# Optimization experiments

Hardware: AMD Instinct MI355X
Metric: run time of the kernel (lower is better)

## Reference

```python
import jax, jax.numpy as jnp
import numpy as np

N = 50000      # nodes
E = 800000     # edges (before self-loops)
F_IN = 128     # num_node_features
G = 128        # number of graphs in batch
NEG_SLOPE = 0.2  # PyG GATConv leaky_relu slope


def _add_self_loops(src, dst, n):
    loop = jnp.arange(n, dtype=src.dtype)
    return jnp.concatenate([src, loop]), jnp.concatenate([dst, loop])


def gcn_conv(x, W, b, src, dst, n):
    h = x @ W
    deg = jax.ops.segment_sum(jnp.ones_like(dst, dtype=h.dtype), dst, num_segments=n)
    dinv = jnp.where(deg > 0, jax.lax.rsqrt(deg), 0.0)
    norm = dinv[src] * dinv[dst]                      # [E+N]
    msg = h[src] * norm[:, None]                      # gather + scale
    return jax.ops.segment_sum(msg, dst, num_segments=n) + b


def gat_conv(x, W, att_src, att_dst, b, src, dst, n, heads, ch):
    # PyG GATConv (concat=True, self-loops added by caller)
    h = (x @ W).reshape(n, heads, ch)                 # [N,H,C]
    a_src = (h * att_src).sum(-1)                     # [N,H]
    a_dst = (h * att_dst).sum(-1)                     # [N,H]
    e = jax.nn.leaky_relu(a_src[src] + a_dst[dst], NEG_SLOPE)  # [E+N,H]
    # segment softmax over edges grouped by destination
    m = jax.ops.segment_max(e, dst, num_segments=n)   # [N,H]
    ex = jnp.exp(e - m[dst])
    s = jax.ops.segment_sum(ex, dst, num_segments=n)  # [N,H]
    alpha = ex / s[dst]                               # [E+N,H]
    msg = h[src] * alpha[:, :, None]                  # [E+N,H,C]
    out = jax.ops.segment_sum(msg, dst, num_segments=n)
    return out.reshape(n, heads * ch) + b


def setup_inputs() -> dict:
    key = jax.random.key(0)
    ks = jax.random.split(key, 16)
    p = lambda k, shape: jax.random.normal(k, shape, jnp.float32) * 0.05
    return {
        "x": jax.random.normal(ks[0], (N, F_IN), jnp.float32),
        "edge_index": jax.random.randint(ks[1], (2, E), 0, N, dtype=jnp.int32),
        "batch": jnp.sort(jax.random.randint(ks[2], (N,), 0, G, dtype=jnp.int32)),
        "W1": p(ks[3], (F_IN, 16)), "b1": jnp.zeros((16,), jnp.float32),
        "W2": p(ks[4], (16, 32)), "b2": jnp.zeros((32,), jnp.float32),
        "W3": p(ks[5], (32, 4 * 32)), "att_src3": p(ks[6], (4, 32)), "att_dst3": p(ks[7], (4, 32)), "b3": jnp.zeros((128,), jnp.float32),
        "W4": p(ks[8], (128, 8 * 32)), "att_src4": p(ks[9], (8, 32)), "att_dst4": p(ks[10], (8, 32)), "b4": jnp.zeros((256,), jnp.float32),
        "Wfc1": p(ks[11], (432, 128)), "bfc1": jnp.zeros((128,), jnp.float32),
        "Wfc2": p(ks[12], (128, 1)), "bfc2": jnp.zeros((1,), jnp.float32),
    }


def reference(x, edge_index, batch, W1, b1, W2, b2, W3, att_src3, att_dst3, b3,
              W4, att_src4, att_dst4, b4, Wfc1, bfc1, Wfc2, bfc2):
    src, dst = _add_self_loops(edge_index[0], edge_index[1], N)
    x1 = jax.nn.relu(gcn_conv(x, W1, b1, src, dst, N))
    x2 = jax.nn.relu(gcn_conv(x1, W2, b2, src, dst, N))
    x3 = jax.nn.relu(gat_conv(x2, W3, att_src3, att_dst3, b3, src, dst, N, 4, 32))
    x4 = jax.nn.relu(gat_conv(x3, W4, att_src4, att_dst4, b4, src, dst, N, 8, 32))
    x_jump = jnp.concatenate([x1, x2, x3, x4], axis=-1)   # [N,432]
    # global mean pool over graphs
    sums = jax.ops.segment_sum(x_jump, batch, num_segments=G)
    cnt = jax.ops.segment_sum(jnp.ones((N,), x_jump.dtype), batch, num_segments=G)
    x_pool = sums / jnp.maximum(cnt, 1.0)[:, None]         # [G,432]
    h = jax.nn.relu(x_pool @ Wfc1 + bfc1)
    return (h @ Wfc2 + bfc2).flatten()                     # [G]
```

## Files before the change

kernel.cpp:

```cpp
#include <hip/hip_runtime.h>
#include <hip/hip_bf16.h>

#define NN 50000
#define NE 800000
#define NG 128
#define EB ((NE + 255)/256)
#define MB1 ((NN + 15)/16)
#define PB 54
#define WB4 128

typedef unsigned short u16;
typedef unsigned int u32;
typedef unsigned char u8;
typedef float f32x4 __attribute__((ext_vector_type(4)));
typedef short s16x8 __attribute__((ext_vector_type(8)));

__device__ __forceinline__ float lrelu(float x){ return x > 0.f ? x : 0.2f*x; }
__device__ __forceinline__ u16 f2bf(float f){
    __hip_bfloat16 h = __float2bfloat16(f);
    return *(u16*)&h;
}
__device__ __forceinline__ void unpack8(uint4 t, float* f){
    f[0]=__uint_as_float(t.x<<16); f[1]=__uint_as_float(t.x&0xffff0000u);
    f[2]=__uint_as_float(t.y<<16); f[3]=__uint_as_float(t.y&0xffff0000u);
    f[4]=__uint_as_float(t.z<<16); f[5]=__uint_as_float(t.z&0xffff0000u);
    f[6]=__uint_as_float(t.w<<16); f[7]=__uint_as_float(t.w&0xffff0000u);
}
__device__ __forceinline__ void ub8(uint2 t, float* f){
    f[0]=(float)(t.x & 0xffu);      f[1]=(float)((t.x>>8) & 0xffu);
    f[2]=(float)((t.x>>16) & 0xffu); f[3]=(float)(t.x>>24);
    f[4]=(float)(t.y & 0xffu);      f[5]=(float)((t.y>>8) & 0xffu);
    f[6]=(float)((t.y>>16) & 0xffu); f[7]=(float)(t.y>>24);
}

__global__ void k_cm(const int* __restrict__ dstE, int* __restrict__ degi,
                     const float* __restrict__ x, const float* __restrict__ W1,
                     const float* __restrict__ W3, const float* __restrict__ W4,
                     const float* __restrict__ as3, const float* __restrict__ ad3,
                     u16* __restrict__ h1, float* __restrict__ pool,
                     u16* __restrict__ W4p, float* __restrict__ asd3){
    if (blockIdx.x < EB){
        int e = blockIdx.x*256 + threadIdx.x;
        if (e < NE) atomicAdd(&degi[dstE[e]], 1);
        return;
    }
    if (blockIdx.x >= EB + MB1){
        int b2 = blockIdx.x - EB - MB1;
        if (b2 < PB){
            int idx = b2*1024 + threadIdx.x*4;
            if (idx < NG*432) *(float4*)(pool + idx) = make_float4(0.f,0.f,0.f,0.f);
        } else if (b2 < PB + WB4){
            int e = (b2 - PB)*256 + threadIdx.x;
            int k = e >> 8, n = e & 255;
            W4p[(k>>3)*2048 + n*8 + (k&7)] = f2bf(W4[e]);
        } else {
            int t = threadIdx.x;
            int t2 = t & 127;
            int h = t2 >> 5, k = t2 & 31;
            const float* av = (t < 128) ? as3 : ad3;
            float v = 0.f;
#pragma unroll
            for (int c = 0; c < 32; c++)
                v += W3[k*128 + h*32 + c] * av[h*32 + c];
            asd3[t] = v;
        }
        return;
    }
    __shared__ float wlT[16][132];
    __shared__ float xs[16][132];
    int node0 = (blockIdx.x - EB) * 16;
    for (int i = threadIdx.x; i < 2048; i += 256){
        int k = i >> 4, m = i & 15;
        wlT[m][k] = W1[i];
    }
    for (int i = threadIdx.x; i < 512; i += 256){
        int r = i >> 5, c = i & 31;
        *(float4*)&xs[r][c*4] = ((const float4*)(x + (size_t)(node0 + r)*128))[c];
    }
    __syncthreads();
    int m  = threadIdx.x & 15;
    int nl = threadIdx.x >> 4;
    float acc = 0.f;
#pragma unroll
    for (int k4 = 0; k4 < 32; k4++){
        float4 xv = *(const float4*)&xs[nl][k4*4];
        float4 wv = *(const float4*)&wlT[m][k4*4];
        acc += xv.x*wv.x + xv.y*wv.y + xv.z*wv.z + xv.w*wv.w;
    }
    h1[(size_t)(node0 + nl)*16 + m] = f2bf(acc);
}

__global__ void k_scan_a(const int* __restrict__ deg, int* __restrict__ rowptr,
                         float* __restrict__ dinv, int* __restrict__ cursor,
                         int* __restrict__ bsum, int n){
    __shared__ int lds[256];
    int base = blockIdx.x*1024 + threadIdx.x*4;
    int v[4]; int s = 0;
#pragma unroll
    for (int k=0;k<4;k++){ v[k] = (base+k < n) ? deg[base+k] : 0; s += v[k]; }
    lds[threadIdx.x] = s;
    __syncthreads();
    for (int off=1; off<256; off<<=1){
        int t = (threadIdx.x>=off) ? lds[threadIdx.x-off] : 0;
        __syncthreads(); lds[threadIdx.x] += t; __syncthreads();
    }
    int run = lds[threadIdx.x] - s;
#pragma unroll
    for (int k=0;k<4;k++){
        if (base+k < n){
            rowptr[base+k] = run;
            dinv[base+k] = rsqrtf((float)(v[k] + 1));
            cursor[base+k] = 0;
        }
        run += v[k];
    }
    if (threadIdx.x == 255) bsum[blockIdx.x] = lds[255];
}

__global__ void k_scan_c(int* __restrict__ rowptr, const int* __restrict__ bsum,
                         int nb, int n){
    __shared__ int off_s;
    if (threadIdx.x < 64){
        int v = ((int)threadIdx.x < nb && (int)threadIdx.x < (int)blockIdx.x)
                ? bsum[threadIdx.x] : 0;
        for (int m=1; m<64; m<<=1) v += __shfl_xor(v, m, 64);
        if (threadIdx.x == 0) off_s = v;
    }
    __syncthreads();
    int o = off_s;
    int idx = blockIdx.x*1024 + threadIdx.x*4;
#pragma unroll
    for (int k=0;k<4;k++) if (idx+k < n) rowptr[idx+k] += o;
    if ((int)blockIdx.x == nb-1 && threadIdx.x == 0) rowptr[n] = o + bsum[nb-1];
}

__global__ void k_scatter(const int* __restrict__ src, const int* __restrict__ dst,
                          const int* __restrict__ rowptr, int* __restrict__ cursor,
                          int* __restrict__ csr_src, int E){
    int e = blockIdx.x*blockDim.x + threadIdx.x;
    if (e < E){
        int d = dst[e];
        int pos = rowptr[d] + atomicAdd(&cursor[d], 1);
        csr_src[pos] = src[e];
    }
}

__global__ void k_gcn_agg16_mm2(const u16* __restrict__ h1, const float* __restrict__ dinv,
                                const int* __restrict__ rowptr, const int* __restrict__ csr_src,
                                const float* __restrict__ b1, const float* __restrict__ W2,
                                const int* __restrict__ batch, float* __restrict__ pool,
                                u16* __restrict__ h2, int n){
    __shared__ float w2s[16*32];
    __shared__ float x1s[16][17];
    __shared__ int gbuf[16];
    for (int i = threadIdx.x; i < 512; i += 256) w2s[i] = W2[i];
    int lin = threadIdx.x & 15;
    int nl  = threadIdx.x >> 4;
    int i = blockIdx.x*16 + nl;
    int ll = lin & 1, slot = lin >> 1;
    float di = dinv[i];
    float acc[8] = {0.f,0.f,0.f,0.f,0.f,0.f,0.f,0.f};
    if (slot == 0){
        uint4 t = *(const uint4*)(h1 + (size_t)i*16 + ll*8);
        float f[8]; unpack8(t, f);
#pragma unroll
        for (int k=0;k<8;k++) acc[k] = di*f[k];
    }
    int e0 = rowptr[i], e1 = rowptr[i+1];
    int e = e0 + slot;
    for (; e + 8 < e1; e += 16){
        int j0 = csr_src[e], j1 = csr_src[e+8];
        float d0 = dinv[j0], d1 = dinv[j1];
        uint4 t0 = *(const uint4*)(h1 + (size_t)j0*16 + ll*8);
        uint4 t1 = *(const uint4*)(h1 + (size_t)j1*16 + ll*8);
        float f0[8], f1[8]; unpack8(t0, f0); unpack8(t1, f1);
#pragma unroll
        for (int k=0;k<8;k++) acc[k] += d0*f0[k] + d1*f1[k];
    }
    if (e < e1){
        int j = csr_src[e];
        float dj = dinv[j];
        uint4 t = *(const uint4*)(h1 + (size_t)j*16 + ll*8);
        float f[8]; unpack8(t, f);
#pragma unroll
        for (int k=0;k<8;k++) acc[k] += dj*f[k];
    }
#pragma unroll
    for (int m = 2; m < 16; m <<= 1){
#pragma unroll
        for (int k=0;k<8;k++) acc[k] += __shfl_xor(acc[k], m, 64);
    }
    if (slot == 0){
#pragma unroll
        for (int k=0;k<8;k++)
            x1s[nl][ll*8+k] = fmaxf(di*acc[k] + b1[ll*8+k], 0.f);
        if (lin == 0) gbuf[nl] = batch[i];
    }
    __syncthreads();
    {
        float a0 = 0.f, a1 = 0.f;
        int m0 = lin*2;
#pragma unroll
        for (int k=0;k<16;k++){
            float xv = x1s[nl][k];
            a0 += xv * w2s[k*32 + m0];
            a1 += xv * w2s[k*32 + m0 + 1];
        }
        u32 pk = (u32)f2bf(a0) | ((u32)f2bf(a1) << 16);
        *(u32*)(h2 + (size_t)i*32 + m0) = pk;
    }
    if (threadIdx.x < 16){
        int c = threadIdx.x;
        int curg = gbuf[0];
        float a = 0.f;
        for (int nd = 0; nd < 16; nd++){
            int g = gbuf[nd];
            if (g != curg){ atomicAdd(&pool[curg*432 + c], a); a = 0.f; curg = g; }
            a += x1s[nd][c];
        }
        atomicAdd(&pool[curg*432 + c], a);
    }
}

__global__ void k_gcn_agg32(const u16* __restrict__ h2, const float* __restrict__ dinv,
                            const int* __restrict__ rowptr, const int* __restrict__ csr_src,
                            const float* __restrict__ b2, const int* __restrict__ batch,
                            const float* __restrict__ asd3, float* __restrict__ pool,
                            u16* __restrict__ x2b, float* __restrict__ asrc3,
                            float* __restrict__ adst3, int n){
    __shared__ float x2s[16][33];
    __shared__ float asdS[256];
    __shared__ int gbuf[16];
    asdS[threadIdx.x] = asd3[threadIdx.x];
    int lin = threadIdx.x & 15;
    int nl  = threadIdx.x >> 4;
    int i = blockIdx.x*16 + nl;
    int ll = lin & 3, slot = lin >> 2;
    float di = dinv[i];
    float acc[8] = {0.f,0.f,0.f,0.f,0.f,0.f,0.f,0.f};
    if (slot == 0){
        uint4 t = *(const uint4*)(h2 + (size_t)i*32 + ll*8);
        float f[8]; unpack8(t, f);
#pragma unroll
        for (int k=0;k<8;k++) acc[k] = di*f[k];
    }
    int e0 = rowptr[i], e1 = rowptr[i+1];
    int e = e0 + slot;
    for (; e + 12 < e1; e += 16){
        int j0 = csr_src[e], j1 = csr_src[e+4], j2 = csr_src[e+8], j3 = csr_src[e+12];
        float d0 = dinv[j0], d1 = dinv[j1], d2 = dinv[j2], d3 = dinv[j3];
        uint4 t0 = *(const uint4*)(h2 + (size_t)j0*32 + ll*8);
        uint4 t1 = *(const uint4*)(h2 + (size_t)j1*32 + ll*8);
        uint4 t2 = *(const uint4*)(h2 + (size_t)j2*32 + ll*8);
        uint4 t3 = *(const uint4*)(h2 + (size_t)j3*32 + ll*8);
        float f0[8], f1[8], f2[8], f3[8];
        unpack8(t0, f0); unpack8(t1, f1); unpack8(t2, f2); unpack8(t3, f3);
#pragma unroll
        for (int k=0;k<8;k++) acc[k] += d0*f0[k] + d1*f1[k] + d2*f2[k] + d3*f3[k];
    }
    for (; e < e1; e += 4){
        int j = csr_src[e];
        float dj = dinv[j];
        uint4 t = *(const uint4*)(h2 + (size_t)j*32 + ll*8);
        float f[8]; unpack8(t, f);
#pragma unroll
        for (int k=0;k<8;k++) acc[k] += dj*f[k];
    }
#pragma unroll
    for (int m = 4; m < 16; m <<= 1){
#pragma unroll
        for (int k=0;k<8;k++) acc[k] += __shfl_xor(acc[k], m, 64);
    }
    if (slot == 0){
        float o[8];
#pragma unroll
        for (int k=0;k<8;k++){
            o[k] = fmaxf(di*acc[k] + b2[ll*8+k], 0.f);
            x2s[nl][ll*8+k] = o[k];
        }
        uint4 pk;
        pk.x = (u32)f2bf(o[0]) | ((u32)f2bf(o[1])<<16);
        pk.y = (u32)f2bf(o[2]) | ((u32)f2bf(o[3])<<16);
        pk.z = (u32)f2bf(o[4]) | ((u32)f2bf(o[5])<<16);
        pk.w = (u32)f2bf(o[6]) | ((u32)f2bf(o[7])<<16);
        *(uint4*)(x2b + (size_t)i*32 + ll*8) = pk;
        if (lin == 0) gbuf[nl] = batch[i];
    }
    __syncthreads();
    if (threadIdx.x < 32){
        int c = threadIdx.x;
        int curg = gbuf[0];
        float a = 0.f;
        for (int nd = 0; nd < 16; nd++){
            int g = gbuf[nd];
            if (g != curg){ atomicAdd(&pool[curg*432 + 16 + c], a); a = 0.f; curg = g; }
            a += x2s[nd][c];
        }
        atomicAdd(&pool[curg*432 + 16 + c], a);
    } else if (threadIdx.x < 160){
        int t = threadIdx.x - 32;
        int nd = t >> 3, r = t & 7;
        int h = r & 3;
        const float* A = &asdS[(r >= 4 ? 128 : 0) + h*32];
        float v = 0.f;
#pragma unroll
        for (int k = 0; k < 32; k++) v += x2s[nd][k] * A[k];
        int node = blockIdx.x*16 + nd;
        if (r >= 4) adst3[(size_t)node*4 + h] = v;
        else        asrc3[(size_t)node*4 + h] = v;
    }
}

__global__ void k_gat_agg3(const u16* __restrict__ x2b, const float* __restrict__ asrc,
                           const float* __restrict__ adst, const int* __restrict__ rowptr,
                           const int* __restrict__ csr_src, const float* __restrict__ W3,
                           const float* __restrict__ b, const int* __restrict__ batch,
                           float* __restrict__ pool, u16* __restrict__ x3b, int n){
    __shared__ float W3s[32][128];
    __shared__ float aggS[4][4][32];
    __shared__ float x3s[4][128];
    __shared__ int gbuf[4];
    int tid = threadIdx.x;
    for (int idx = tid; idx < 4096; idx += 256)
        W3s[idx >> 7][idx & 127] = W3[idx];
    int lane = tid & 63;
    int wid  = tid >> 6;
    int i = blockIdx.x*4 + wid;
    int ll   = lane & 15;
    int slot = lane >> 4;
    int head = ll >> 2;
    int kseg = (ll & 3) * 8;
    float ad = adst[(size_t)i*4 + head];
    float acc[8] = {0.f,0.f,0.f,0.f,0.f,0.f,0.f,0.f};
    float s = 0.f;
    if (slot == 0){
        float w = __expf(lrelu(asrc[(size_t)i*4 + head] + ad));
        uint4 t = *(const uint4*)(x2b + (size_t)i*32 + kseg);
        float f[8]; unpack8(t, f);
#pragma unroll
        for (int k=0;k<8;k++) acc[k] = w*f[k];
        s = w;
    }
    int e0 = rowptr[i], e1 = rowptr[i+1];
    int e = e0 + slot;
    for (; e + 12 < e1; e += 16){
        int j0 = csr_src[e], j1 = csr_src[e+4], j2 = csr_src[e+8], j3 = csr_src[e+12];
        float w0 = __expf(lrelu(asrc[(size_t)j0*4 + head] + ad));
        float w1 = __expf(lrelu(asrc[(size_t)j1*4 + head] + ad));
        float w2 = __expf(lrelu(asrc[(size_t)j2*4 + head] + ad));
        float w3 = __expf(lrelu(asrc[(size_t)j3*4 + head] + ad));
        uint4 t0 = *(const uint4*)(x2b + (size_t)j0*32 + kseg);
        uint4 t1 = *(const uint4*)(x2b + (size_t)j1*32 + kseg);
        uint4 t2 = *(const uint4*)(x2b + (size_t)j2*32 + kseg);
        uint4 t3 = *(const uint4*)(x2b + (size_t)j3*32 + kseg);
        float f0[8], f1[8], f2[8], f3[8];
        unpack8(t0, f0); unpack8(t1, f1); unpack8(t2, f2); unpack8(t3, f3);
#pragma unroll
        for (int k=0;k<8;k++) acc[k] += w0*f0[k] + w1*f1[k] + w2*f2[k] + w3*f3[k];
        s += w0 + w1 + w2 + w3;
    }
    for (; e < e1; e += 4){
        int j = csr_src[e];
        float w = __expf(lrelu(asrc[(size_t)j*4 + head] + ad));
        uint4 t = *(const uint4*)(x2b + (size_t)j*32 + kseg);
        float f[8]; unpack8(t, f);
#pragma unroll
        for (int k=0;k<8;k++) acc[k] += w*f[k];
        s += w;
    }
#pragma unroll
    for (int m = 16; m < 64; m <<= 1){
        s += __shfl_xor(s, m, 64);
#pragma unroll
        for (int k=0;k<8;k++) acc[k] += __shfl_xor(acc[k], m, 64);
    }
    if (slot == 0){
        float inv = 1.f / s;
        float o[8];
#pragma unroll
        for (int k=0;k<8;k++) o[k] = acc[k]*inv;
        *(float4*)&aggS[wid][head][kseg]     = make_float4(o[0],o[1],o[2],o[3]);
        *(float4*)&aggS[wid][head][kseg + 4] = make_float4(o[4],o[5],o[6],o[7]);
        if (ll == 0) gbuf[wid] = batch[i];
    }
    __syncthreads();
    {
        int c0 = lane*2;
        const float* ag = aggS[wid][lane >> 4];
        float a0 = 0.f, a1 = 0.f;
#pragma unroll
        for (int k = 0; k < 32; k++){
            float av = ag[k];
            a0 += av * W3s[k][c0];
            a1 += av * W3s[k][c0+1];
        }
        float o0 = fmaxf(a0 + b[c0],   0.f);
        float o1 = fmaxf(a1 + b[c0+1], 0.f);
        x3s[wid][c0] = o0; x3s[wid][c0+1] = o1;
        u32 pk = (u32)f2bf(o0) | ((u32)f2bf(o1) << 16);
        *(u32*)(x3b + (size_t)i*128 + c0) = pk;
    }
    __syncthreads();
    if (tid < 128){
        int c = tid;
        int g0 = gbuf[0];
        float sum = 0.f;
#pragma unroll
        for (int wd = 0; wd < 4; wd++){
            float v = x3s[wd][c];
            int gw = gbuf[wd];
            if (gw == g0) sum += v;
            else atomicAdd(&pool[gw*432 + 48 + c], v);
        }
        atomicAdd(&pool[g0*432 + 48 + c], sum);
    }
}

__global__ void k_mm4_mfma(const u16* __restrict__ x3b, const u16* __restrict__ W4p,
                           const float* __restrict__ as, const float* __restrict__ adt,
                           u8* __restrict__ hb, float* __restrict__ scl,
                           float* __restrict__ asrc, float* __restrict__ adst){
    __shared__ u16 outS[64][136];
    __shared__ float asS[128], adS[128];
    int tid = threadIdx.x;
    int lane = tid & 63, w = tid >> 6;
    int cbase = blockIdx.x * 128;
    int nbase = blockIdx.y * 64;
    if (tid < 128){ asS[tid] = as[cbase + tid]; adS[tid] = adt[cbase + tid]; }
    int q = lane >> 4, r16 = lane & 15;
    int m = nbase + w*16 + r16;
    f32x4 acc[8] = {};
    for (int s = 0; s < 4; s++){
        s16x8 af = (s16x8){0,0,0,0,0,0,0,0};
        if (m < NN) af = *(const s16x8*)(x3b + (size_t)m*128 + s*32 + q*8);
        int kb = s*4 + q;
#pragma unroll
        for (int t = 0; t < 8; t++){
            s16x8 bf = *(const s16x8*)(W4p + (size_t)kb*2048 + (cbase + t*16 + r16)*8);
            acc[t] = __builtin_amdgcn_mfma_f32_16x16x32_bf16(af, bf, acc[t], 0, 0, 0);
        }
    }
#pragma unroll
    for (int t = 0; t < 8; t++){
#pragma unroll
        for (int r = 0; r < 4; r++){
            outS[w*16 + q*4 + r][t*16 + r16] = f2bf(acc[t][r]);
        }
    }
    __syncthreads();
    {
        int row = w*16 + r16;
        int node = nbase + row;
        float ps = 0.f, pd = 0.f, mx = 0.f;
        const u16* orow = &outS[row][q*32];
#pragma unroll
        for (int c = 0; c < 32; c++){
            float f = __uint_as_float(((u32)orow[c]) << 16);
            ps += f * asS[q*32 + c];
            pd += f * adS[q*32 + c];
            mx = fmaxf(mx, fabsf(f));
        }
        if (node < NN){
            int hg = (cbase >> 5) + q;
            asrc[(size_t)node*8 + hg] = ps;
            adst[(size_t)node*8 + hg] = pd;
        }
        mx = fmaxf(mx, __shfl_xor(mx, 16, 64));
        mx = fmaxf(mx, __shfl_xor(mx, 32, 64));
        float inv = mx > 0.f ? 127.f/mx : 0.f;
        if (node < NN && q == 0) scl[(size_t)node*2 + (cbase>>7)] = mx * (1.f/127.f);
        if (node < NN){
            u32 pk_[8];
#pragma unroll
            for (int g = 0; g < 8; g++){
                u32 v = 0;
#pragma unroll
                for (int kk = 0; kk < 4; kk++){
                    float f = __uint_as_float(((u32)orow[g*4+kk]) << 16);
                    int bq = (int)rintf(f*inv) + 128;
                    v |= ((u32)bq) << (8*kk);
                }
                pk_[g] = v;
            }
            *(uint4*)(hb + (size_t)node*256 + cbase + q*32)      = make_uint4(pk_[0],pk_[1],pk_[2],pk_[3]);
            *(uint4*)(hb + (size_t)node*256 + cbase + q*32 + 16) = make_uint4(pk_[4],pk_[5],pk_[6],pk_[7]);
        }
    }
}

__global__ void k_gat_agg4(const u8* __restrict__ h, const float* __restrict__ scl,
                           const float* __restrict__ asrc, const float* __restrict__ adst,
                           const int* __restrict__ rowptr, const int* __restrict__ csr_src,
                           const float* __restrict__ b, const int* __restrict__ batch,
                           float* __restrict__ pool){
    constexpr int S = 2;
    __shared__ float x4buf[4][256];
    __shared__ int gbuf[4];
    int lane = threadIdx.x & 63;
    int wid  = threadIdx.x >> 6;
    int i = blockIdx.x*4 + wid;
    int ll   = lane & 31;
    int slot = lane >> 5;
    int head = ll >> 2;
    int half = ll >> 4;
    float ad = adst[(size_t)i*8 + head];
    float acc[8] = {0.f,0.f,0.f,0.f,0.f,0.f,0.f,0.f};
    float s = 0.f, cw = 0.f;
    if (slot == 0){
        float w = __expf(lrelu(asrc[(size_t)i*8 + head] + ad));
        float ws = w * scl[(size_t)i*2 + half];
        uint2 t = *(const uint2*)(h + (size_t)i*256 + ll*8);
        float f[8]; ub8(t, f);
#pragma unroll
        for (int k=0;k<8;k++) acc[k] = ws*f[k];
        s = w; cw = ws;
    }
    int e0 = rowptr[i], e1 = rowptr[i+1];
    int e = e0 + slot;
    for (; e + 3*S < e1; e += 4*S){
        int j0 = csr_src[e], j1 = csr_src[e+S], j2 = csr_src[e+2*S], j3 = csr_src[e+3*S];
        float w0 = __expf(lrelu(asrc[(size_t)j0*8 + head] + ad));
        float w1 = __expf(lrelu(asrc[(size_t)j1*8 + head] + ad));
        float w2 = __expf(lrelu(asrc[(size_t)j2*8 + head] + ad));
        float w3 = __expf(lrelu(asrc[(size_t)j3*8 + head] + ad));
        float ws0 = w0 * scl[(size_t)j0*2 + half];
        float ws1 = w1 * scl[(size_t)j1*2 + half];
        float ws2 = w2 * scl[(size_t)j2*2 + half];
        float ws3 = w3 * scl[(size_t)j3*2 + half];
        uint2 t0 = *(const uint2*)(h + (size_t)j0*256 + ll*8);
        uint2 t1 = *(const uint2*)(h + (size_t)j1*256 + ll*8);
        uint2 t2 = *(const uint2*)(h + (size_t)j2*256 + ll*8);
        uint2 t3 = *(const uint2*)(h + (size_t)j3*256 + ll*8);
        float f0[8], f1[8], f2[8], f3[8];
        ub8(t0, f0); ub8(t1, f1); ub8(t2, f2); ub8(t3, f3);
#pragma unroll
        for (int k=0;k<8;k++) acc[k] += ws0*f0[k] + ws1*f1[k] + ws2*f2[k] + ws3*f3[k];
        s += w0 + w1 + w2 + w3;
        cw += ws0 + ws1 + ws2 + ws3;
    }
    for (; e < e1; e += S){
        int j = csr_src[e];
        float w = __expf(lrelu(asrc[(size_t)j*8 + head] + ad));
        float ws = w * scl[(size_t)j*2 + half];
        uint2 t = *(const uint2*)(h + (size_t)j*256 + ll*8);
        float f[8]; ub8(t, f);
#pragma unroll
        for (int k=0;k<8;k++) acc[k] += ws*f[k];
        s += w; cw += ws;
    }
#pragma unroll
    for (int k=0;k<8;k++) acc[k] -= 128.f*cw;
    s += __shfl_xor(s, 32, 64);
#pragma unroll
    for (int k=0;k<8;k++) acc[k] += __shfl_xor(acc[k], 32, 64);
    if (slot == 0){
        float inv = 1.f / s;
#pragma unroll
        for (int k=0;k<8;k++)
            x4buf[wid][ll*8+k] = fmaxf(acc[k]*inv + b[ll*8+k], 0.f);
        if (ll == 0) gbuf[wid] = batch[i];
    }
    __syncthreads();
    {
        int c = threadIdx.x;
        int g0 = gbuf[0];
        float sum = 0.f;
#pragma unroll
        for (int wd = 0; wd < 4; wd++){
            float v = x4buf[wd][c];
            int gw = gbuf[wd];
            if (gw == g0) sum += v;
            else atomicAdd(&pool[gw*432 + 176 + c], v);
        }
        atomicAdd(&pool[g0*432 + 176 + c], sum);
    }
}

__global__ void k_fc(const float* __restrict__ pool, const int* __restrict__ batch,
                     const float* __restrict__ Wf1, const float* __restrict__ bf1,
                     const float* __restrict__ Wf2, const float* __restrict__ bf2,
                     float* __restrict__ out){
    int g = blockIdx.x, j = threadIdx.x;
    int lo = 0, hi = NN;
    while (lo < hi){ int mid = (lo+hi) >> 1; if (batch[mid] < g) lo = mid+1; else hi = mid; }
    int s0 = lo;
    lo = 0; hi = NN;
    while (lo < hi){ int mid = (lo+hi) >> 1; if (batch[mid] < g+1) lo = mid+1; else hi = mid; }
    int cnt = lo - s0;
    float invc = 1.f / (float)max(cnt, 1);
    float acc = 0.f;
    for (int k = 0; k < 432; k++) acc += pool[g*432 + k] * Wf1[k*128 + j];
    float hv = fmaxf(acc * invc + bf1[j], 0.f);
    float p = hv * Wf2[j];
    for (int off = 32; off > 0; off >>= 1) p += __shfl_down(p, off, 64);
    __shared__ float part[2];
    if ((j & 63) == 0) part[j >> 6] = p;
    __syncthreads();
    if (j == 0) out[g] = part[0] + part[1] + bf2[0];
}

extern "C" void kernel_launch(void* const* d_in, const int* in_sizes, int n_in,
                              void* d_out, int out_size, void* d_ws, size_t ws_size,
                              hipStream_t stream){
    const float* x     = (const float*)d_in[0];
    const int*   ei    = (const int*)  d_in[1];
    const int*   batch = (const int*)  d_in[2];
    const float* W1 = (const float*)d_in[3];  const float* b1 = (const float*)d_in[4];
    const float* W2 = (const float*)d_in[5];  const float* b2 = (const float*)d_in[6];
    const float* W3 = (const float*)d_in[7];
    const float* as3 = (const float*)d_in[8]; const float* ad3 = (const float*)d_in[9];
    const float* b3 = (const float*)d_in[10];
    const float* W4 = (const float*)d_in[11];
    const float* as4 = (const float*)d_in[12]; const float* ad4 = (const float*)d_in[13];
    const float* b4 = (const float*)d_in[14];
    const float* Wf1 = (const float*)d_in[15]; const float* bf1 = (const float*)d_in[16];
    const float* Wf2 = (const float*)d_in[17]; const float* bf2 = (const float*)d_in[18];
    float* out = (float*)d_out;

    const int* srcE = ei;
    const int* dstE = ei + NE;

    char* base = (char*)d_ws; size_t off = 0;
    auto alloc = [&](size_t bytes)->void*{
        void* p = base + off;
        off += (bytes + 255) & ~(size_t)255;
        return p;
    };
    int*   degi    = (int*)  alloc((size_t)NN*4);
    int*   cursor  = (int*)  alloc((size_t)NN*4);
    float* dinv    = (float*)alloc((size_t)NN*4);
    int*   rowptr  = (int*)  alloc((size_t)(NN+1)*4);
    int*   bsum    = (int*)  alloc(64*4);
    int*   csr_src = (int*)  alloc((size_t)NE*4);
    u16*   h1b     = (u16*)  alloc((size_t)NN*16*2);
    u16*   h2b     = (u16*)  alloc((size_t)NN*32*2);
    u8*    hb4     = (u8*)   alloc((size_t)NN*256);
    float* scl4    = (float*)alloc((size_t)NN*2*4);
    u16*   x2b     = (u16*)  alloc((size_t)NN*32*2);
    u16*   x3b     = (u16*)  alloc((size_t)NN*128*2);
    u16*   W4p     = (u16*)  alloc((size_t)32768*2);
    float* asd3    = (float*)alloc(256*4);
    float* a_src   = (float*)alloc((size_t)NN*8*4);
    float* a_dst   = (float*)alloc((size_t)NN*8*4);
    float* pool    = (float*)alloc((size_t)NG*432*4);

    hipMemsetAsync(degi, 0, (size_t)NN*4, stream);

    const int SB = (NN + 1023)/1024;

    k_cm     <<<EB + MB1 + PB + WB4 + 1, 256, 0, stream>>>(dstE, degi, x, W1, W3, W4,
                                                           as3, ad3, h1b, pool, W4p, asd3);
    k_scan_a <<<SB, 256, 0, stream>>>(degi, rowptr, dinv, cursor, bsum, NN);
    k_scan_c <<<SB, 256, 0, stream>>>(rowptr, bsum, SB, NN);
    k_scatter<<<EB, 256, 0, stream>>>(srcE, dstE, rowptr, cursor, csr_src, NE);

    k_gcn_agg16_mm2<<<NN/16, 256, 0, stream>>>(h1b, dinv, rowptr, csr_src, b1, W2,
                                               batch, pool, h2b, NN);

    k_gcn_agg32<<<NN/16, 256, 0, stream>>>(h2b, dinv, rowptr, csr_src, b2, batch,
                                           asd3, pool, x2b, a_src, a_dst, NN);

    k_gat_agg3<<<NN/4, 256, 0, stream>>>(x2b, a_src, a_dst, rowptr, csr_src, W3, b3,
                                         batch, pool, x3b, NN);

    {
        dim3 grid(2, (NN + 63)/64);
        k_mm4_mfma<<<grid, 256, 0, stream>>>(x3b, W4p, as4, ad4, hb4, scl4, a_src, a_dst);
    }
    k_gat_agg4<<<NN/4, 256, 0, stream>>>(hb4, scl4, a_src, a_dst, rowptr, csr_src, b4,
                                         batch, pool);

    k_fc<<<NG, 128, 0, stream>>>(pool, batch, Wf1, bf1, Wf2, bf2, out);
}
```

Measured before the change: 375.0 us.

## Process four nodes per wave in GAT layer-3 aggregation to amortize W3 staging

Each wave now handles four destination nodes sequentially instead of one, so each block covers 16 nodes and the grid shrinks fourfold. This amortizes the 16KB W3 shared-memory load across more nodes. The per-node aggregated vector is broadcast through wave shuffles rather than a shared buffer, which removes the two block barriers after the gather. Pooling is reduced per wave in registers before the atomics. In exchange there are fewer blocks and the four nodes in a wave run serially, which may lower the number of gathers in flight at once.

```diff
diff --git a/kernel.cpp b/kernel.cpp
--- a/kernel.cpp
+++ b/kernel.cpp
@@ -317,103 +317,99 @@
                            const float* __restrict__ b, const int* __restrict__ batch,
                            float* __restrict__ pool, u16* __restrict__ x3b, int n){
     __shared__ float W3s[32][128];
-    __shared__ float aggS[4][4][32];
-    __shared__ float x3s[4][128];
-    __shared__ int gbuf[4];
     int tid = threadIdx.x;
     for (int idx = tid; idx < 4096; idx += 256)
         W3s[idx >> 7][idx & 127] = W3[idx];
+    __syncthreads();
     int lane = tid & 63;
     int wid  = tid >> 6;
-    int i = blockIdx.x*4 + wid;
     int ll   = lane & 15;
     int slot = lane >> 4;
     int head = ll >> 2;
     int kseg = (ll & 3) * 8;
-    float ad = adst[(size_t)i*4 + head];
-    float acc[8] = {0.f,0.f,0.f,0.f,0.f,0.f,0.f,0.f};
-    float s = 0.f;
-    if (slot == 0){
-        float w = __expf(lrelu(asrc[(size_t)i*4 + head] + ad));
-        uint4 t = *(const uint4*)(x2b + (size_t)i*32 + kseg);
-        float f[8]; unpack8(t, f);
-#pragma unroll
-        for (int k=0;k<8;k++) acc[k] = w*f[k];
-        s = w;
-    }
-    int e0 = rowptr[i], e1 = rowptr[i+1];
-    int e = e0 + slot;
-    for (; e + 12 < e1; e += 16){
-        int j0 = csr_src[e], j1 = csr_src[e+4], j2 = csr_src[e+8], j3 = csr_src[e+12];
-        float w0 = __expf(lrelu(asrc[(size_t)j0*4 + head] + ad));
-        float w1 = __expf(lrelu(asrc[(size_t)j1*4 + head] + ad));
-        float w2 = __expf(lrelu(asrc[(size_t)j2*4 + head] + ad));
-        float w3 = __expf(lrelu(asrc[(size_t)j3*4 + head] + ad));
-        uint4 t0 = *(const uint4*)(x2b + (size_t)j0*32 + kseg);
-        uint4 t1 = *(const uint4*)(x2b + (size_t)j1*32 + kseg);
-        uint4 t2 = *(const uint4*)(x2b + (size_t)j2*32 + kseg);
-        uint4 t3 = *(const uint4*)(x2b + (size_t)j3*32 + kseg);
-        float f0[8], f1[8], f2[8], f3[8];
-        unpack8(t0, f0); unpack8(t1, f1); unpack8(t2, f2); unpack8(t3, f3);
-#pragma unroll
-        for (int k=0;k<8;k++) acc[k] += w0*f0[k] + w1*f1[k] + w2*f2[k] + w3*f3[k];
-        s += w0 + w1 + w2 + w3;
-    }
-    for (; e < e1; e += 4){
-        int j = csr_src[e];
-        float w = __expf(lrelu(asrc[(size_t)j*4 + head] + ad));
-        uint4 t = *(const uint4*)(x2b + (size_t)j*32 + kseg);
-        float f[8]; unpack8(t, f);
-#pragma unroll
-        for (int k=0;k<8;k++) acc[k] += w*f[k];
-        s += w;
-    }
-#pragma unroll
-    for (int m = 16; m < 64; m <<= 1){
-        s += __shfl_xor(s, m, 64);
-#pragma unroll
-        for (int k=0;k<8;k++) acc[k] += __shfl_xor(acc[k], m, 64);
-    }
-    if (slot == 0){
+    int c0   = lane * 2;
+    int ph   = lane >> 4;
+    float bc0 = b[c0], bc1 = b[c0+1];
+    float o_r[4][2];
+    int   g_r[4];
+    int ibase = blockIdx.x * 16 + wid * 4;
+#pragma unroll
+    for (int t = 0; t < 4; t++){
+        int i = ibase + t;
+        float ad = adst[(size_t)i*4 + head];
+        float acc[8] = {0.f,0.f,0.f,0.f,0.f,0.f,0.f,0.f};
+        float s = 0.f;
+        if (slot == 0){
+            float w = __expf(lrelu(asrc[(size_t)i*4 + head] + ad));
+            uint4 tq = *(const uint4*)(x2b + (size_t)i*32 + kseg);
+            float f[8]; unpack8(tq, f);
+#pragma unroll
+            for (int k=0;k<8;k++) acc[k] = w*f[k];
+            s = w;
+        }
+        int e0 = rowptr[i], e1 = rowptr[i+1];
+        int e = e0 + slot;
+        for (; e + 12 < e1; e += 16){
+            int j0 = csr_src[e], j1 = csr_src[e+4], j2 = csr_src[e+8], j3 = csr_src[e+12];
+            float w0 = __expf(lrelu(asrc[(size_t)j0*4 + head] + ad));
+            float w1 = __expf(lrelu(asrc[(size_t)j1*4 + head] + ad));
+            float w2 = __expf(lrelu(asrc[(size_t)j2*4 + head] + ad));
+            float w3 = __expf(lrelu(asrc[(size_t)j3*4 + head] + ad));
+            uint4 t0 = *(const uint4*)(x2b + (size_t)j0*32 + kseg);
+            uint4 t1 = *(const uint4*)(x2b + (size_t)j1*32 + kseg);
+            uint4 t2 = *(const uint4*)(x2b + (size_t)j2*32 + kseg);
+            uint4 t3 = *(const uint4*)(x2b + (size_t)j3*32 + kseg);
+            float f0[8], f1[8], f2[8], f3[8];
+            unpack8(t0, f0); unpack8(t1, f1); unpack8(t2, f2); unpack8(t3, f3);
+#pragma unroll
+            for (int k=0;k<8;k++) acc[k] += w0*f0[k] + w1*f1[k] + w2*f2[k] + w3*f3[k];
+            s += w0 + w1 + w2 + w3;
+        }
+        for (; e < e1; e += 4){
+            int j = csr_src[e];
+            float w = __expf(lrelu(asrc[(size_t)j*4 + head] + ad));
+            uint4 tq = *(const uint4*)(x2b + (size_t)j*32 + kseg);
+            float f[8]; unpack8(tq, f);
+#pragma unroll
+            for (int k=0;k<8;k++) acc[k] += w*f[k];
+            s += w;
+        }
+#pragma unroll
+        for (int m = 16; m < 64; m <<= 1){
+            s += __shfl_xor(s, m, 64);
+#pragma unroll
+            for (int k=0;k<8;k++) acc[k] += __shfl_xor(acc[k], m, 64);
+        }
         float inv = 1.f / s;
-        float o[8];
-#pragma unroll
-        for (int k=0;k<8;k++) o[k] = acc[k]*inv;
-        *(float4*)&aggS[wid][head][kseg]     = make_float4(o[0],o[1],o[2],o[3]);
-        *(float4*)&aggS[wid][head][kseg + 4] = make_float4(o[4],o[5],o[6],o[7]);
-        if (ll == 0) gbuf[wid] = batch[i];
-    }
-    __syncthreads();
-    {
-        int c0 = lane*2;
-        const float* ag = aggS[wid][lane >> 4];
+#pragma unroll
+        for (int k=0;k<8;k++) acc[k] *= inv;
         float a0 = 0.f, a1 = 0.f;
 #pragma unroll
         for (int k = 0; k < 32; k++){
-            float av = ag[k];
+            float av = __shfl(acc[k & 7], ph*4 + (k >> 3), 64);
             a0 += av * W3s[k][c0];
             a1 += av * W3s[k][c0+1];
         }
-        float o0 = fmaxf(a0 + b[c0],   0.f);
-        float o1 = fmaxf(a1 + b[c0+1], 0.f);
-        x3s[wid][c0] = o0; x3s[wid][c0+1] = o1;
+        float o0 = fmaxf(a0 + bc0, 0.f);
+        float o1 = fmaxf(a1 + bc1, 0.f);
+        o_r[t][0] = o0; o_r[t][1] = o1;
+        g_r[t] = batch[i];
         u32 pk = (u32)f2bf(o0) | ((u32)f2bf(o1) << 16);
         *(u32*)(x3b + (size_t)i*128 + c0) = pk;
     }
-    __syncthreads();
-    if (tid < 128){
-        int c = tid;
-        int g0 = gbuf[0];
-        float sum = 0.f;
-#pragma unroll
-        for (int wd = 0; wd < 4; wd++){
-            float v = x3s[wd][c];
-            int gw = gbuf[wd];
-            if (gw == g0) sum += v;
-            else atomicAdd(&pool[gw*432 + 48 + c], v);
-        }
-        atomicAdd(&pool[g0*432 + 48 + c], sum);
-    }
+    float s0 = o_r[0][0], s1 = o_r[0][1];
+    int cg = g_r[0];
+#pragma unroll
+    for (int t = 1; t < 4; t++){
+        if (g_r[t] != cg){
+            atomicAdd(&pool[cg*432 + 48 + c0],     s0);
+            atomicAdd(&pool[cg*432 + 48 + c0 + 1], s1);
+            s0 = 0.f; s1 = 0.f; cg = g_r[t];
+        }
+        s0 += o_r[t][0]; s1 += o_r[t][1];
+    }
+    atomicAdd(&pool[cg*432 + 48 + c0],     s0);
+    atomicAdd(&pool[cg*432 + 48 + c0 + 1], s1);
 }
 
 __global__ void k_mm4_mfma(const u16* __restrict__ x3b, const u16* __restrict__ W4p,
@@ -660,8 +656,8 @@
     k_gcn_agg32<<<NN/16, 256, 0, stream>>>(h2b, dinv, rowptr, csr_src, b2, batch,
                                            asd3, pool, x2b, a_src, a_dst, NN);
 
-    k_gat_agg3<<<NN/4, 256, 0, stream>>>(x2b, a_src, a_dst, rowptr, csr_src, W3, b3,
-                                         batch, pool, x3b, NN);
+    k_gat_agg3<<<NN/16, 256, 0, stream>>>(x2b, a_src, a_dst, rowptr, csr_src, W3, b3,
+                                          batch, pool, x3b, NN);
 
     {
         dim3 grid(2, (NN + 63)/64);
```

New measurement: 386.6 us. 3.1% more time.
